# Kernel tuning notes

Hardware: AMD Instinct MI355X
Metric: run time of the kernel (lower is better)

Reference implementation:

```python
import jax, jax.numpy as jnp
import numpy as np

D_MODEL = 1024
N_HEADS = 16
HEAD_DIM = D_MODEL // N_HEADS
NEG_INF = -1e30


def _rotary(v):
    # v: [B, H, T, hd]. Original module rotates each (even, odd) pair by 90 deg:
    # out[..., 2i] = -v[..., 2i+1]; out[..., 2i+1] = v[..., 2i]
    v2 = v.reshape(*v.shape[:-1], HEAD_DIM // 2, 2)
    return jnp.stack([-v2[..., 1], v2[..., 0]], axis=-1).reshape(v.shape)


def setup_inputs() -> dict:
    key = jax.random.key(0)
    ks = jax.random.split(key, 9)
    B, T, D = 2, 2048, D_MODEL
    s = 1.0 / np.sqrt(D)
    inp = {
        "x": jax.random.normal(ks[0], (B, T, D), dtype=jnp.float32),
        "Wq_w": jax.random.normal(ks[1], (D, D), dtype=jnp.float32) * s,
        "Wq_b": jnp.zeros((D,), dtype=jnp.float32),
        "Wk_w": jax.random.normal(ks[2], (D, D), dtype=jnp.float32) * s,
        "Wk_b": jnp.zeros((D,), dtype=jnp.float32),
        "Wv_w": jax.random.normal(ks[3], (D, D), dtype=jnp.float32) * s,
        "Wv_b": jnp.zeros((D,), dtype=jnp.float32),
        "Wo_w": jax.random.normal(ks[4], (D, D), dtype=jnp.float32) * s,
        "Wo_b": jnp.zeros((D,), dtype=jnp.float32),
    }
    # create_sparse_mask: block-diagonal True windows of size T//4
    window = T // 4
    blk = jnp.arange(T) // window
    inp["sparse_mask"] = blk[:, None] == blk[None, :]
    return inp


def reference(x, Wq_w, Wq_b, Wk_w, Wk_b, Wv_w, Wv_b, Wo_w, Wo_b, sparse_mask):
    B, T, D = x.shape
    H, hd = N_HEADS, HEAD_DIM

    def proj(w, b):  # [B,T,D] -> [B,H,T,hd]
        return (x @ w.T + b).reshape(B, T, H, hd).transpose(0, 2, 1, 3)

    q = _rotary(proj(Wq_w, Wq_b))
    k = _rotary(proj(Wk_w, Wk_b))
    v = proj(Wv_w, Wv_b)

    scores = jnp.einsum("bhqd,bhkd->bhqk", q, k) / jnp.sqrt(jnp.asarray(hd, x.dtype))
    causal = jnp.tril(jnp.ones((T, T), dtype=bool))
    allowed = sparse_mask & causal  # block-diagonal AND causal
    scores = jnp.where(allowed, scores, NEG_INF)
    attn = jax.nn.softmax(scores, axis=-1)  # dropout_p=0.1 omitted (eval mode)
    out = jnp.einsum("bhqk,bhkd->bhqd", attn, v)
    out = out.transpose(0, 2, 1, 3).reshape(B, T, D)
    return out @ Wo_w.T + Wo_b
```

## Files before the change

kernel.cpp:

```cpp
#include <hip/hip_runtime.h>
#include <hip/hip_bf16.h>
#include <stdint.h>

typedef __attribute__((ext_vector_type(4))) float f32x4;
typedef __attribute__((ext_vector_type(8))) __bf16 bf16x8;
typedef __attribute__((ext_vector_type(4))) unsigned short u16x4;
typedef __attribute__((ext_vector_type(8))) unsigned short u16x8;
typedef const __attribute__((address_space(1))) void* as1_cvp;
typedef __attribute__((address_space(3))) void* as3_vp;

#define LOG2E 1.44269504088896340736f

#define VMW0() asm volatile("s_waitcnt vmcnt(0)" ::: "memory")
#define VMW2() asm volatile("s_waitcnt vmcnt(2)" ::: "memory")
#define VMW3() asm volatile("s_waitcnt vmcnt(3)" ::: "memory")
#define VMW4() asm volatile("s_waitcnt vmcnt(4)" ::: "memory")
#define VMW5() asm volatile("s_waitcnt vmcnt(5)" ::: "memory")
#define VMW6() asm volatile("s_waitcnt vmcnt(6)" ::: "memory")
#define BAR()  do { __builtin_amdgcn_sched_barrier(0); __builtin_amdgcn_s_barrier(); \
                    __builtin_amdgcn_sched_barrier(0); } while (0)

static __device__ __forceinline__ unsigned short f2bf(float f) {
  union { float f; unsigned int u; } c; c.f = f;
  unsigned int r = c.u + 0x7FFFu + ((c.u >> 16) & 1u);
  return (unsigned short)(r >> 16);
}

static __device__ __forceinline__ void gl_lds16(const void* g, void* l) {
  __builtin_amdgcn_global_load_lds((as1_cvp)(uintptr_t)g, (as3_vp)(uintptr_t)l, 16, 0, 0);
}

__global__ __launch_bounds__(256) void cvt_kernel(
    const float* __restrict__ x, const float* __restrict__ wq, const float* __restrict__ wk,
    const float* __restrict__ wv, const float* __restrict__ wo,
    unsigned short* __restrict__ xb, unsigned short* __restrict__ wqb,
    unsigned short* __restrict__ wkb, unsigned short* __restrict__ wvb,
    unsigned short* __restrict__ wob) {
  long e = ((long)blockIdx.x * 256 + threadIdx.x) * 8;
  const float* s; unsigned short* d; long o;
  if (e < 4194304)      { s = x;  d = xb;  o = e; }
  else if (e < 5242880) { s = wq; d = wqb; o = e - 4194304; }
  else if (e < 6291456) { s = wk; d = wkb; o = e - 5242880; }
  else if (e < 7340032) { s = wv; d = wvb; o = e - 6291456; }
  else                  { s = wo; d = wob; o = e - 7340032; }
  float4 a = *(const float4*)(s + o);
  float4 b = *(const float4*)(s + o + 4);
  u16x8 v;
  v[0] = f2bf(a.x); v[1] = f2bf(a.y); v[2] = f2bf(a.z); v[3] = f2bf(a.w);
  v[4] = f2bf(b.x); v[5] = f2bf(b.y); v[6] = f2bf(b.z); v[7] = f2bf(b.w);
  *(u16x8*)(d + o) = v;
}

__global__ __launch_bounds__(512, 2) void gemm_qkv8(
    const unsigned short* __restrict__ xb, const unsigned short* __restrict__ wcat,
    const float* __restrict__ bq, const float* __restrict__ bk, const float* __restrict__ bv,
    unsigned short* __restrict__ qo, unsigned short* __restrict__ ko,
    unsigned short* __restrict__ vto) {
  __shared__ __align__(16) char lds[114688];
  const int tid = threadIdx.x;
  const int lane = tid & 63, wid = tid >> 6;
  const int wm = wid >> 2, wn = wid & 3;
  const int c = lane & 15, g = lane >> 4;

  const int bid = blockIdx.x;
  const int swz = (bid & 7) * 32 + (bid >> 3);
  const int n0 = (swz & 15) * 192;
  const int m0 = (swz >> 4) << 8;

  const int srow = tid >> 3;
  const int coff = (((tid & 7) ^ (srow & 7)) << 4);
  const char* Ab = (const char*)xb;
  const char* Bb = (const char*)wcat;

  const int swzr0 = ((g ^ (c & 7)) << 4);
  const int swzr1 = (((4 | g) ^ (c & 7)) << 4);

  f32x4 acc[8][3] = {};
  bf16x8 aa[2][2], bbf[3][2];

  auto STAGE = [&](int kt, int unit) {
    char* db = lds + (kt & 1) * 57344;
    const char* gp; char* dst;
    if (unit < 3) {
      gp = Bb + ((long)(n0 + unit * 64 + srow) << 11) + (kt << 7) + coff;
      dst = db + 32768 + unit * 8192 + tid * 16;
    } else {
      const int u = unit - 3;
      gp = Ab + ((long)(m0 + u * 64 + srow) << 11) + (kt << 7) + coff;
      dst = db + u * 8192 + tid * 16;
    }
    gl_lds16(gp, dst);
  };
  auto RDA = [&](int bufb, int u) {
    const char* p = lds + bufb + (u << 13) + (((wm << 5) + c) << 7);
#pragma unroll
    for (int f = 0; f < 2; ++f) {
      aa[f][0] = *(const bf16x8*)(p + (f << 11) + swzr0);
      aa[f][1] = *(const bf16x8*)(p + (f << 11) + swzr1);
    }
  };
  auto RDB = [&](int bufb) {
#pragma unroll
    for (int nf = 0; nf < 3; ++nf) {
      const int rB = wn * 48 + (nf << 4) + c;
      const char* p = lds + bufb + 32768 + ((rB >> 6) << 13) + ((rB & 63) << 7);
      bbf[nf][0] = *(const bf16x8*)(p + swzr0);
      bbf[nf][1] = *(const bf16x8*)(p + swzr1);
    }
  };
  auto MM = [&](int u) {
    __builtin_amdgcn_s_setprio(1);
#pragma unroll
    for (int f = 0; f < 2; ++f)
#pragma unroll
      for (int nf = 0; nf < 3; ++nf)
#pragma unroll
        for (int kf = 0; kf < 2; ++kf)
          acc[u * 2 + f][nf] = __builtin_amdgcn_mfma_f32_16x16x32_bf16(
              aa[f][kf], bbf[nf][kf], acc[u * 2 + f][nf], 0, 0, 0);
    __builtin_amdgcn_s_setprio(0);
  };

#pragma unroll
  for (int u = 0; u < 7; ++u) STAGE(0, u);
  VMW3();
  BAR();

  for (int kt = 0; kt < 16; ++kt) {
    const int bufb = (kt & 1) * 57344;
    RDB(bufb); RDA(bufb, 0);
    STAGE(kt + 1, 0); STAGE(kt + 1, 1);
    VMW4(); BAR();
    MM(0);
    RDA(bufb, 1);
    STAGE(kt + 1, 2); STAGE(kt + 1, 3);
    VMW5(); BAR();
    MM(1);
    RDA(bufb, 2);
    STAGE(kt + 1, 4); STAGE(kt + 1, 5);
    VMW6(); BAR();
    MM(2);
    RDA(bufb, 3);
    STAGE(kt + 1, 6);
    VMW3(); BAR();
    MM(3);
  }
  VMW0();

#pragma unroll
  for (int nf = 0; nf < 3; ++nf) {
    const int n = n0 + wn * 48 + (nf << 4) + c;
    const int z = n >> 10, nn = n & 1023;
    const float bb_ = (z == 0 ? bq : z == 1 ? bk : bv)[nn];
    const float sc = (z == 0) ? 0.125f : 1.0f;
    const int h = nn >> 6, dd = nn & 63;
#pragma unroll
    for (int a = 0; a < 8; ++a) {
      const int mb = m0 + ((a >> 1) << 6) + (wm << 5) + ((a & 1) << 4) + (g << 2);
      const int b = mb >> 11, tt = mb & 2047;
      if (z < 2) {
        unsigned short* dst = (z == 0 ? qo : ko) +
            ((((long)(b << 4) + h) << 11) + tt) * 64 + dd;
#pragma unroll
        for (int j = 0; j < 4; ++j) dst[(long)j * 64] = f2bf((acc[a][nf][j] + bb_) * sc);
      } else {
        u16x4 pk;
#pragma unroll
        for (int j = 0; j < 4; ++j) pk[j] = f2bf(acc[a][nf][j] + bb_);
        *(u16x4*)(vto + ((((long)((b << 4) + h) << 6) + dd) << 11) + tt) = pk;
      }
    }
  }
}

static __device__ __forceinline__ void gemm128_core(
    const unsigned short* A, const unsigned short* W, int m0, int n0,
    f32x4 (&acc)[4][4], char* lds_a, char* lds_b) {
  const int tid = threadIdx.x;
  const int lane = tid & 63, wv_ = tid >> 6;
  const int wr = wv_ >> 1, wc = wv_ & 1;
  const int c = lane & 15, g = lane >> 4;
  const int srow = tid >> 2;
  const int scol = (tid & 3) << 4;
  const char* aG = (const char*)A + (((long)(m0 + srow)) << 11) + scol;
  const char* bG = (const char*)W + (((long)(n0 + srow)) << 11) + scol;

  for (int kt = 0; kt < 32; ++kt) {
    const long ko = (long)kt << 6;
    gl_lds16(aG + ko,                 lds_a + tid * 16);
    gl_lds16(aG + ko + (64l << 11),   lds_a + 4096 + tid * 16);
    gl_lds16(bG + ko,                 lds_b + tid * 16);
    gl_lds16(bG + ko + (64l << 11),   lds_b + 4096 + tid * 16);
    __syncthreads();

    bf16x8 af[4], bfr[4];
#pragma unroll
    for (int mf = 0; mf < 4; ++mf)
      af[mf] = *(const bf16x8*)(lds_a + (((wr << 6) + (mf << 4) + c) << 6) + (g << 4));
#pragma unroll
    for (int nf = 0; nf < 4; ++nf)
      bfr[nf] = *(const bf16x8*)(lds_b + (((wc << 6) + (nf << 4) + c) << 6) + (g << 4));
#pragma unroll
    for (int mf = 0; mf < 4; ++mf)
#pragma unroll
      for (int nf = 0; nf < 4; ++nf)
        acc[mf][nf] = __builtin_amdgcn_mfma_f32_16x16x32_bf16(af[mf], bfr[nf], acc[mf][nf], 0, 0, 0);
    __syncthreads();
  }
}

__global__ __launch_bounds__(512) void attn_kernel(
    const unsigned short* __restrict__ qg, const unsigned short* __restrict__ kg,
    const unsigned short* __restrict__ vtg, unsigned short* __restrict__ og) {
  __shared__ __align__(16) char kv_s[2][16384];
  __shared__ __align__(16) char p_s[8][2304];

  const int bx = blockIdx.x, bh = blockIdx.y;
  const int qt = ((bx & 3) << 2) + 3 - (bx >> 2);
  const int tid = threadIdx.x;
  const int lane = tid & 63, w = tid >> 6;
  const int c = lane & 15, g = lane >> 4;
  const int q0 = qt << 7;
  const int wstart = q0 & ~511;
  const int nt = ((q0 - wstart) >> 6) + 2;

  const unsigned short* qrow = qg + (((long)bh << 11) + q0 + (w << 4) + c) * 64;
  bf16x8 qa0 = *(const bf16x8*)(qrow + (g << 3));
  bf16x8 qa1 = *(const bf16x8*)(qrow + (g << 3) + 32);

  float m_run = -3.0e38f, l_run = 0.0f;
  f32x4 oacc[4] = {};

  const int sr = tid >> 3;
  const int jx16 = (((tid & 7) ^ (sr & 7)) << 4);
  const char* kbase = (const char*)kg + ((((long)bh << 11) + sr) << 7) + jx16;
  const char* vbase = (const char*)vtg + ((((long)bh << 6) + sr) << 12) + jx16;
  const int t16 = tid << 4;

  auto STAGEKV = [&](int kv0, int bsel) {
    char* dst = kv_s[bsel];
    gl_lds16(kbase + ((long)kv0 << 7), dst + t16);
    gl_lds16(vbase + ((long)kv0 << 1), dst + 8192 + t16);
  };

  STAGEKV(wstart, 0);

  for (int t = 0; t < nt; ++t) {
    if (t + 1 < nt) {
      STAGEKV(wstart + ((t + 1) << 6), (t + 1) & 1);
      VMW2();
    } else {
      VMW0();
    }
    BAR();

    const char* kb_ = kv_s[t & 1];
    const char* vb_ = kv_s[t & 1] + 8192;
    const int kv0 = wstart + (t << 6);

    f32x4 sacc[4] = {};
    __builtin_amdgcn_s_setprio(1);
#pragma unroll
    for (int mf = 0; mf < 4; ++mf) {
      const int kr = (mf << 4) + c;
      const char* kp = kb_ + (kr << 7);
      bf16x8 k0 = *(const bf16x8*)(kp + ((g ^ (kr & 7)) << 4));
      bf16x8 k1 = *(const bf16x8*)(kp + (((4 | g) ^ (kr & 7)) << 4));
      sacc[mf] = __builtin_amdgcn_mfma_f32_16x16x32_bf16(k0, qa0, sacc[mf], 0, 0, 0);
      sacc[mf] = __builtin_amdgcn_mfma_f32_16x16x32_bf16(k1, qa1, sacc[mf], 0, 0, 0);
    }
    __builtin_amdgcn_s_setprio(0);

    const int dkv = kv0 - q0;
    if (dkv > (w << 4) - 64) {
      const int qrel = (w << 4) + c;
#pragma unroll
      for (int mf = 0; mf < 4; ++mf)
#pragma unroll
        for (int j = 0; j < 4; ++j)
          if (dkv + (mf << 4) + (g << 2) + j > qrel) sacc[mf][j] = -3.0e38f;
    }

    float pmax = -3.0e38f;
#pragma unroll
    for (int mf = 0; mf < 4; ++mf)
#pragma unroll
      for (int j = 0; j < 4; ++j) pmax = fmaxf(pmax, sacc[mf][j]);
    pmax = fmaxf(pmax, __shfl_xor(pmax, 16));
    pmax = fmaxf(pmax, __shfl_xor(pmax, 32));

    const float m_new = fmaxf(m_run, pmax);
    float lsum = 0.0f;
#pragma unroll
    for (int mf = 0; mf < 4; ++mf)
#pragma unroll
      for (int j = 0; j < 4; ++j) {
        const float p = __builtin_amdgcn_exp2f((sacc[mf][j] - m_new) * LOG2E);
        sacc[mf][j] = p;
        lsum += p;
      }
    lsum += __shfl_xor(lsum, 16);
    lsum += __shfl_xor(lsum, 32);
    const float alpha = __builtin_amdgcn_exp2f((m_run - m_new) * LOG2E);
    l_run = l_run * alpha + lsum;
    m_run = m_new;

    {
      char* pw = p_s[w] + c * 144;
#pragma unroll
      for (int mf = 0; mf < 4; ++mf) {
        u16x4 pk;
#pragma unroll
        for (int j = 0; j < 4; ++j) pk[j] = f2bf(sacc[mf][j]);
        *(u16x4*)(pw + (mf << 5) + (g << 3)) = pk;
      }
    }

#pragma unroll
    for (int j = 0; j < 4; ++j) {
      const float aj = __shfl(alpha, (g << 2) + j);
#pragma unroll
      for (int nf = 0; nf < 4; ++nf) oacc[nf][j] *= aj;
    }

    const char* pr = p_s[w] + c * 144;
    __builtin_amdgcn_s_setprio(1);
#pragma unroll
    for (int kk = 0; kk < 2; ++kk) {
      bf16x8 pa = *(const bf16x8*)(pr + (kk << 6) + (g << 4));
#pragma unroll
      for (int nf = 0; nf < 4; ++nf) {
        const int vr = (nf << 4) + c;
        bf16x8 vb = *(const bf16x8*)(vb_ + (vr << 7) +
                                     ((((kk << 2) | g) ^ (vr & 7)) << 4));
        oacc[nf] = __builtin_amdgcn_mfma_f32_16x16x32_bf16(pa, vb, oacc[nf], 0, 0, 0);
      }
    }
    __builtin_amdgcn_s_setprio(0);
    BAR();
  }

  const int b = bh >> 4, h = bh & 15;
#pragma unroll
  for (int j = 0; j < 4; ++j) {
    const float linv = 1.0f / __shfl(l_run, (g << 2) + j);
    const int trow = q0 + (w << 4) + (g << 2) + j;
    unsigned short* dst = og + ((((long)(b << 11)) + trow) << 10) + (h << 6);
#pragma unroll
    for (int nf = 0; nf < 4; ++nf)
      dst[(nf << 4) + c] = f2bf(oacc[nf][j] * linv);
  }
}

__global__ __launch_bounds__(256) void gemm_oproj(
    const unsigned short* __restrict__ ab, const unsigned short* __restrict__ wob,
    const float* __restrict__ bo, float* __restrict__ out) {
  __shared__ __align__(16) char lds_a[8192];
  __shared__ __align__(16) char lds_b[8192];
  const int n0 = blockIdx.x << 7, m0 = blockIdx.y << 7;
  f32x4 acc[4][4] = {};
  gemm128_core(ab, wob, m0, n0, acc, lds_a, lds_b);

  const int tid = threadIdx.x, lane = tid & 63, wv_ = tid >> 6;
  const int wr = wv_ >> 1, wc = wv_ & 1, c = lane & 15, g = lane >> 4;
#pragma unroll
  for (int nf = 0; nf < 4; ++nf) {
    const int n = n0 + (wc << 6) + (nf << 4) + c;
    const float bb = bo[n];
#pragma unroll
    for (int mf = 0; mf < 4; ++mf) {
      const int mb = m0 + (wr << 6) + (mf << 4) + (g << 2);
#pragma unroll
      for (int j = 0; j < 4; ++j)
        out[((long)(mb + j) << 10) + n] = acc[mf][nf][j] + bb;
    }
  }
}

extern "C" void kernel_launch(void* const* d_in, const int* in_sizes, int n_in,
                              void* d_out, int out_size, void* d_ws, size_t ws_size,
                              hipStream_t stream) {
  const float* x  = (const float*)d_in[0];
  const float* wq = (const float*)d_in[1];
  const float* bq = (const float*)d_in[2];
  const float* wk = (const float*)d_in[3];
  const float* bk = (const float*)d_in[4];
  const float* wv = (const float*)d_in[5];
  const float* bv = (const float*)d_in[6];
  const float* wo = (const float*)d_in[7];
  const float* bo = (const float*)d_in[8];

  char* ws = (char*)d_ws;
  unsigned short* xb    = (unsigned short*)(ws);
  unsigned short* wqb   = (unsigned short*)(ws + 8388608);
  unsigned short* wkb   = (unsigned short*)(ws + 10485760);
  unsigned short* wvb   = (unsigned short*)(ws + 12582912);
  unsigned short* wob   = (unsigned short*)(ws + 14680064);
  unsigned short* qb    = (unsigned short*)(ws + 16777216);
  unsigned short* kb    = (unsigned short*)(ws + 25165824);
  unsigned short* vtb   = (unsigned short*)(ws + 33554432);
  unsigned short* attnb = xb;

  cvt_kernel<<<4096, 256, 0, stream>>>(x, wq, wk, wv, wo, xb, wqb, wkb, wvb, wob);
  gemm_qkv8<<<256, 512, 0, stream>>>(xb, wqb, bq, bk, bv, qb, kb, vtb);
  attn_kernel<<<dim3(16, 32), 512, 0, stream>>>(qb, kb, vtb, attnb);
  gemm_oproj<<<dim3(8, 32), 256, 0, stream>>>(attnb, wob, bo, (float*)d_out);
}
```

Baseline: 86.27 us.

## Rewrite output projection GEMM with 8-wave double-buffered pipeline; triple-buffer attention KV

Replaces the 256-thread output-projection GEMM, which loaded K=64 slices with a full barrier each step, with a 512-thread kernel. The new kernel stages K=128 tiles into swizzled, double-buffered LDS, overlaps global-to-LDS loads with MFMA work in half-steps, and remaps block indices for cache locality. The attention kernel moves from double to triple buffering of K/V tiles so loads run two tiles ahead. The cost is more LDS per block (64KB for the GEMM, an extra 16KB for attention), which may reduce occupancy.

```diff
diff --git a/kernel.cpp b/kernel.cpp
--- a/kernel.cpp
+++ b/kernel.cpp
@@ -12,6 +12,7 @@
 #define LOG2E 1.44269504088896340736f
 
 #define VMW0() asm volatile("s_waitcnt vmcnt(0)" ::: "memory")
+#define VMW1() asm volatile("s_waitcnt vmcnt(1)" ::: "memory")
 #define VMW2() asm volatile("s_waitcnt vmcnt(2)" ::: "memory")
 #define VMW3() asm volatile("s_waitcnt vmcnt(3)" ::: "memory")
 #define VMW4() asm volatile("s_waitcnt vmcnt(4)" ::: "memory")
@@ -173,46 +174,103 @@
   }
 }
 
-static __device__ __forceinline__ void gemm128_core(
-    const unsigned short* A, const unsigned short* W, int m0, int n0,
-    f32x4 (&acc)[4][4], char* lds_a, char* lds_b) {
+__global__ __launch_bounds__(512, 2) void gemm_oproj8(
+    const unsigned short* __restrict__ ab, const unsigned short* __restrict__ wob,
+    const float* __restrict__ bo, float* __restrict__ out) {
+  __shared__ __align__(16) char lds[65536];
   const int tid = threadIdx.x;
-  const int lane = tid & 63, wv_ = tid >> 6;
-  const int wr = wv_ >> 1, wc = wv_ & 1;
+  const int lane = tid & 63, wid = tid >> 6;
+  const int wm = wid >> 2, wn = wid & 3;
   const int c = lane & 15, g = lane >> 4;
-  const int srow = tid >> 2;
-  const int scol = (tid & 3) << 4;
-  const char* aG = (const char*)A + (((long)(m0 + srow)) << 11) + scol;
-  const char* bG = (const char*)W + (((long)(n0 + srow)) << 11) + scol;
-
-  for (int kt = 0; kt < 32; ++kt) {
-    const long ko = (long)kt << 6;
-    gl_lds16(aG + ko,                 lds_a + tid * 16);
-    gl_lds16(aG + ko + (64l << 11),   lds_a + 4096 + tid * 16);
-    gl_lds16(bG + ko,                 lds_b + tid * 16);
-    gl_lds16(bG + ko + (64l << 11),   lds_b + 4096 + tid * 16);
-    __syncthreads();
-
-    bf16x8 af[4], bfr[4];
-#pragma unroll
-    for (int mf = 0; mf < 4; ++mf)
-      af[mf] = *(const bf16x8*)(lds_a + (((wr << 6) + (mf << 4) + c) << 6) + (g << 4));
-#pragma unroll
-    for (int nf = 0; nf < 4; ++nf)
-      bfr[nf] = *(const bf16x8*)(lds_b + (((wc << 6) + (nf << 4) + c) << 6) + (g << 4));
-#pragma unroll
-    for (int mf = 0; mf < 4; ++mf)
-#pragma unroll
-      for (int nf = 0; nf < 4; ++nf)
-        acc[mf][nf] = __builtin_amdgcn_mfma_f32_16x16x32_bf16(af[mf], bfr[nf], acc[mf][nf], 0, 0, 0);
-    __syncthreads();
+
+  const int bid = blockIdx.x;
+  const int swz = (bid & 7) * 32 + (bid >> 3);
+  const int n0 = (swz & 7) << 7;
+  const int m0 = (swz >> 3) << 7;
+
+  const int srow = tid >> 3;
+  const int coff = (((tid & 7) ^ (srow & 7)) << 4);
+  const char* Ab = (const char*)ab;
+  const char* Bb = (const char*)wob;
+
+  const int swzr0 = ((g ^ (c & 7)) << 4);
+  const int swzr1 = (((4 | g) ^ (c & 7)) << 4);
+
+  f32x4 acc[4][2] = {};
+  bf16x8 aa[2][2], bbf[2][2];
+
+  auto STAGE = [&](int kt, int unit) {
+    const int ktc = (kt < 16) ? kt : 15;
+    char* db = lds + (kt & 1) * 32768;
+    const char* gp;
+    if (unit < 2) gp = Ab + ((long)(m0 + unit * 64 + srow) << 11) + (ktc << 7) + coff;
+    else          gp = Bb + ((long)(n0 + (unit - 2) * 64 + srow) << 11) + (ktc << 7) + coff;
+    gl_lds16(gp, db + unit * 8192 + tid * 16);
+  };
+  auto RDA = [&](int bufb, int u) {
+    const char* p = lds + bufb + (((u << 6) + (wm << 5) + c) << 7);
+#pragma unroll
+    for (int f = 0; f < 2; ++f) {
+      aa[f][0] = *(const bf16x8*)(p + (f << 11) + swzr0);
+      aa[f][1] = *(const bf16x8*)(p + (f << 11) + swzr1);
+    }
+  };
+  auto RDB = [&](int bufb) {
+#pragma unroll
+    for (int nf = 0; nf < 2; ++nf) {
+      const char* p = lds + bufb + 16384 + (((nf << 6) + (wn << 4) + c) << 7);
+      bbf[nf][0] = *(const bf16x8*)(p + swzr0);
+      bbf[nf][1] = *(const bf16x8*)(p + swzr1);
+    }
+  };
+  auto MM = [&](int u) {
+    __builtin_amdgcn_s_setprio(1);
+#pragma unroll
+    for (int f = 0; f < 2; ++f)
+#pragma unroll
+      for (int nf = 0; nf < 2; ++nf)
+#pragma unroll
+        for (int kf = 0; kf < 2; ++kf)
+          acc[u * 2 + f][nf] = __builtin_amdgcn_mfma_f32_16x16x32_bf16(
+              aa[f][kf], bbf[nf][kf], acc[u * 2 + f][nf], 0, 0, 0);
+    __builtin_amdgcn_s_setprio(0);
+  };
+
+  STAGE(0, 0); STAGE(0, 2); STAGE(0, 3); STAGE(0, 1);
+  VMW1();
+  BAR();
+
+  for (int kt = 0; kt < 16; ++kt) {
+    const int bufb = (kt & 1) * 32768;
+    RDB(bufb); RDA(bufb, 0);
+    STAGE(kt + 1, 0); STAGE(kt + 1, 2);
+    VMW2(); BAR();
+    MM(0);
+    RDA(bufb, 1);
+    STAGE(kt + 1, 3); STAGE(kt + 1, 1);
+    VMW1(); BAR();
+    MM(1);
+  }
+  VMW0();
+
+#pragma unroll
+  for (int nf = 0; nf < 2; ++nf) {
+    const int n = n0 + (nf << 6) + (wn << 4) + c;
+    const float bb = bo[n];
+#pragma unroll
+    for (int a = 0; a < 4; ++a) {
+      const int mb = m0 + ((a >> 1) << 6) + (wm << 5) + ((a & 1) << 4) + (g << 2);
+#pragma unroll
+      for (int j = 0; j < 4; ++j)
+        out[((long)(mb + j) << 10) + n] = acc[a][nf][j] + bb;
+    }
   }
 }
 
 __global__ __launch_bounds__(512) void attn_kernel(
     const unsigned short* __restrict__ qg, const unsigned short* __restrict__ kg,
     const unsigned short* __restrict__ vtg, unsigned short* __restrict__ og) {
-  __shared__ __align__(16) char kv_s[2][16384];
+  __shared__ __align__(16) char kv_s[3][16384];
   __shared__ __align__(16) char p_s[8][2304];
 
   const int bx = blockIdx.x, bh = blockIdx.y;
@@ -244,18 +302,22 @@
   };
 
   STAGEKV(wstart, 0);
-
+  STAGEKV(wstart + 64, 1);
+
+  int rsel = 0, ssel = 2;
   for (int t = 0; t < nt; ++t) {
-    if (t + 1 < nt) {
-      STAGEKV(wstart + ((t + 1) << 6), (t + 1) & 1);
+    if (t + 2 < nt) {
+      STAGEKV(wstart + ((t + 2) << 6), ssel);
+      VMW4();
+    } else if (t + 1 < nt) {
       VMW2();
     } else {
       VMW0();
     }
     BAR();
 
-    const char* kb_ = kv_s[t & 1];
-    const char* vb_ = kv_s[t & 1] + 8192;
+    const char* kb_ = kv_s[rsel];
+    const char* vb_ = kv_s[rsel] + 8192;
     const int kv0 = wstart + (t << 6);
 
     f32x4 sacc[4] = {};
@@ -338,6 +400,9 @@
     }
     __builtin_amdgcn_s_setprio(0);
     BAR();
+
+    rsel = (rsel == 2) ? 0 : rsel + 1;
+    ssel = (ssel == 2) ? 0 : ssel + 1;
   }
 
   const int b = bh >> 4, h = bh & 15;
@@ -349,31 +414,6 @@
 #pragma unroll
     for (int nf = 0; nf < 4; ++nf)
       dst[(nf << 4) + c] = f2bf(oacc[nf][j] * linv);
-  }
-}
-
-__global__ __launch_bounds__(256) void gemm_oproj(
-    const unsigned short* __restrict__ ab, const unsigned short* __restrict__ wob,
-    const float* __restrict__ bo, float* __restrict__ out) {
-  __shared__ __align__(16) char lds_a[8192];
-  __shared__ __align__(16) char lds_b[8192];
-  const int n0 = blockIdx.x << 7, m0 = blockIdx.y << 7;
-  f32x4 acc[4][4] = {};
-  gemm128_core(ab, wob, m0, n0, acc, lds_a, lds_b);
-
-  const int tid = threadIdx.x, lane = tid & 63, wv_ = tid >> 6;
-  const int wr = wv_ >> 1, wc = wv_ & 1, c = lane & 15, g = lane >> 4;
-#pragma unroll
-  for (int nf = 0; nf < 4; ++nf) {
-    const int n = n0 + (wc << 6) + (nf << 4) + c;
-    const float bb = bo[n];
-#pragma unroll
-    for (int mf = 0; mf < 4; ++mf) {
-      const int mb = m0 + (wr << 6) + (mf << 4) + (g << 2);
-#pragma unroll
-      for (int j = 0; j < 4; ++j)
-        out[((long)(mb + j) << 10) + n] = acc[mf][nf][j] + bb;
-    }
   }
 }
 
@@ -404,5 +444,5 @@
   cvt_kernel<<<4096, 256, 0, stream>>>(x, wq, wk, wv, wo, xb, wqb, wkb, wvb, wob);
   gemm_qkv8<<<256, 512, 0, stream>>>(xb, wqb, bq, bk, bv, qb, kb, vtb);
   attn_kernel<<<dim3(16, 32), 512, 0, stream>>>(qb, kb, vtb, attnb);
-  gemm_oproj<<<dim3(8, 32), 256, 0, stream>>>(attnb, wob, bo, (float*)d_out);
-}
+  gemm_oproj8<<<256, 512, 0, stream>>>(attnb, wob, bo, (float*)d_out);
+}
```

After: 79.27 us. 8.1% less time.
